# Optimization experiments

Hardware: AMD Instinct MI355X
Metric: run time of the kernel (lower is better)

The kernel has to match this reference:

```python
import jax, jax.numpy as jnp
import numpy as np

B_, L_, D_ = 4, 4096, 256
EXPAND = 2
DI_ = EXPAND * D_      # 512 inner channels
H_ = 8                 # heads
P_ = DI_ // H_         # 64 head dim
N_ = 16                # d_state
K_ = 3                 # depthwise conv kernel


def setup_inputs() -> dict:
    key = jax.random.key(0)
    ks = jax.random.split(key, 32)

    def n(i, shape, s=0.02):
        return jax.random.normal(ks[i], shape, jnp.float32) * s

    inp = {"inputs": jax.random.normal(ks[0], (B_, L_, D_), jnp.float32)}
    i = 1
    for pre in ("f_", "b_"):
        inp[pre + "in_proj_w"] = n(i, (2 * DI_, D_)); i += 1
        inp[pre + "in_proj_b"] = jnp.zeros((2 * DI_,), jnp.float32)
        inp[pre + "x_proj_w"] = n(i, (DI_ + 2 * H_ * N_, DI_)); i += 1
        inp[pre + "x_proj_b"] = jnp.zeros((DI_ + 2 * H_ * N_,), jnp.float32)
        inp[pre + "dt_bias"] = jnp.full((DI_,), -4.0, jnp.float32)  # softplus -> small dt
        inp[pre + "A_log"] = jnp.log(jnp.tile(jnp.arange(1, N_ + 1, dtype=jnp.float32), (DI_, 1)))
        inp[pre + "D_skip"] = jnp.ones((DI_,), jnp.float32)
        inp[pre + "out_proj_w"] = n(i, (D_, DI_)); i += 1
        inp[pre + "out_proj_b"] = jnp.zeros((D_,), jnp.float32)
    inp["norm_w"] = jnp.ones((D_,), jnp.float32)
    inp["norm_b"] = jnp.zeros((D_,), jnp.float32)
    inp["conv_w"] = n(20, (D_, 1, K_), 0.1)   # depthwise: (out_ch, in_ch/groups=1, k)
    inp["conv_b"] = jnp.zeros((D_,), jnp.float32)
    return inp


def _layernorm(x, w, b):
    m = x.mean(-1, keepdims=True)
    v = ((x - m) ** 2).mean(-1, keepdims=True)
    return (x - m) * jax.lax.rsqrt(v + 1e-5) * w + b


def _mh_ssm(x, in_w, in_b, xp_w, xp_b, dt_b, A_log, D_skip, out_w, out_b):
    # Multihead selective-scan SSM (Mamba-style). x: (B, L, D)
    Bsz, L, _ = x.shape
    xz = x @ in_w.T + in_b                      # (B, L, 2*DI)
    xi, z = jnp.split(xz, 2, axis=-1)
    xi = jax.nn.silu(xi)                        # (B, L, DI)
    proj = xi @ xp_w.T + xp_b                   # (B, L, DI + 2*H*N)
    dt = jax.nn.softplus(proj[..., :DI_] + dt_b)        # (B, L, DI)
    Bm = proj[..., DI_:DI_ + H_ * N_].reshape(Bsz, L, H_, N_)
    Cm = proj[..., DI_ + H_ * N_:].reshape(Bsz, L, H_, N_)
    A = -jnp.exp(A_log).reshape(H_, P_, N_)     # (H, P, N), negative
    x4 = xi.reshape(Bsz, L, H_, P_)
    dt4 = dt.reshape(Bsz, L, H_, P_)

    def step(h, t):
        xt, dtt, Bt, Ct = t                     # (B,H,P), (B,H,P), (B,H,N), (B,H,N)
        dA = jnp.exp(dtt[..., None] * A)        # (B,H,P,N)
        h = h * dA + dtt[..., None] * Bt[:, :, None, :] * xt[..., None]
        y = jnp.einsum('bhpn,bhn->bhp', h, Ct)
        return h, y

    xs = (x4.transpose(1, 0, 2, 3), dt4.transpose(1, 0, 2, 3),
          Bm.transpose(1, 0, 2, 3), Cm.transpose(1, 0, 2, 3))
    h0 = jnp.zeros((Bsz, H_, P_, N_), x.dtype)
    _, ys = jax.lax.scan(step, h0, xs)          # ys: (L,B,H,P)
    y = ys.transpose(1, 0, 2, 3).reshape(Bsz, L, DI_) + xi * D_skip
    y = y * jax.nn.silu(z)                      # gating
    return y @ out_w.T + out_b                  # (B, L, D)


def reference(inputs,
              f_in_proj_w, f_in_proj_b, f_x_proj_w, f_x_proj_b, f_dt_bias,
              f_A_log, f_D_skip, f_out_proj_w, f_out_proj_b,
              b_in_proj_w, b_in_proj_b, b_x_proj_w, b_x_proj_b, b_dt_bias,
              b_A_log, b_D_skip, b_out_proj_w, b_out_proj_b,
              norm_w, norm_b, conv_w, conv_b):
    # Cascaded bidirectional SSM: backward(flip(norm(forward(x)))) then flip back
    y1 = _mh_ssm(inputs, f_in_proj_w, f_in_proj_b, f_x_proj_w, f_x_proj_b,
                 f_dt_bias, f_A_log, f_D_skip, f_out_proj_w, f_out_proj_b)
    y1n = jnp.flip(_layernorm(y1, norm_w, norm_b), axis=1)
    y2 = _mh_ssm(y1n, b_in_proj_w, b_in_proj_b, b_x_proj_w, b_x_proj_b,
                 b_dt_bias, b_A_log, b_D_skip, b_out_proj_w, b_out_proj_b)
    out = jnp.flip(y2, axis=1)
    # locality branch: depthwise Conv1d (groups=C) + exact GELU
    xt = inputs.transpose(0, 2, 1)              # (B, C, L)
    c = jax.lax.conv_general_dilated(
        xt, conv_w, window_strides=(1,), padding=[(1, 1)],
        dimension_numbers=('NCH', 'OIH', 'NCH'), feature_group_count=D_)
    c = jax.nn.gelu(c + conv_b[None, :, None], approximate=False)
    return out + c.transpose(0, 2, 1)
```

## Files before the change

### kernel.cpp

```cpp
#include <hip/hip_runtime.h>
#include <hip/hip_bf16.h>
#include <cstdint>
#include <cstddef>

#define B_  4
#define L_  4096
#define D_  256
#define DI_ 512
#define H_  8
#define P_  64
#define N_  16
#define M_  (B_ * L_)
#define PROJ_ (DI_ + 2 * H_ * N_)

#define NC_ 128
#define CL_ (L_ / NC_)
#define NSEQ_ (B_ * H_ * P_ * N_)
#define LOG2E_ 1.4426950408889634f

typedef __bf16 bf16x8 __attribute__((ext_vector_type(8)));
typedef float f32x4 __attribute__((ext_vector_type(4)));

__device__ __forceinline__ void cp16_lds(const __hip_bfloat16* g, short* lds) {
    __builtin_amdgcn_global_load_lds(
        (const __attribute__((address_space(1))) void*)g,
        (__attribute__((address_space(3))) void*)lds, 16, 0, 0);
}

#define FS0 (M_ * D_)
#define FS1 (2 * DI_ * D_)
#define FS2 (PROJ_ * DI_)
#define FS3 (D_ * DI_)
#define FC1 (FS0 + FS1)
#define FC2 (FC1 + FS2)
#define FC3 (FC2 + FS3)
#define FC4 (FC3 + FS1)
#define FC5 (FC4 + FS2)
#define FC6 (FC5 + FS3)

__launch_bounds__(256)
__global__ void f2b_all(const float* __restrict__ i0, const float* __restrict__ i1,
                        const float* __restrict__ i2, const float* __restrict__ i3,
                        const float* __restrict__ i4, const float* __restrict__ i5,
                        const float* __restrict__ i6,
                        __hip_bfloat16* o0, __hip_bfloat16* o1, __hip_bfloat16* o2,
                        __hip_bfloat16* o3, __hip_bfloat16* o4, __hip_bfloat16* o5,
                        __hip_bfloat16* o6) {
    for (int idx = blockIdx.x * 256 + threadIdx.x; idx < FC6; idx += gridDim.x * 256) {
        const float* s; __hip_bfloat16* d; int off;
        if (idx < FS0)      { s = i0; d = o0; off = idx; }
        else if (idx < FC1) { s = i1; d = o1; off = idx - FS0; }
        else if (idx < FC2) { s = i2; d = o2; off = idx - FC1; }
        else if (idx < FC3) { s = i3; d = o3; off = idx - FC2; }
        else if (idx < FC4) { s = i4; d = o4; off = idx - FC3; }
        else if (idx < FC5) { s = i5; d = o5; off = idx - FC4; }
        else                { s = i6; d = o6; off = idx - FC5; }
        d[off] = __float2bfloat16(s[off]);
    }
}

template <int EPI>
__launch_bounds__(256)
__global__ void gemm_mfma(const __hip_bfloat16* __restrict__ A,
                          const __hip_bfloat16* __restrict__ W,
                          const float* __restrict__ bias, int Kv,
                          __hip_bfloat16* __restrict__ zb,
                          __hip_bfloat16* __restrict__ obf,
                          const float* __restrict__ aux) {
    __shared__ short As[128 * 64];
    __shared__ short Bs[128 * 64];
    const int tid = threadIdx.x;
    const int lane = tid & 63;
    const int wave = tid >> 6;
    const int bm = blockIdx.x * 128;
    const int bn = blockIdx.y * 128;
    const int wm = (wave >> 1) * 64;
    const int wn = (wave & 1) * 64;

    f32x4 acc[4][4];
#pragma unroll
    for (int i = 0; i < 4; ++i)
#pragma unroll
        for (int j = 0; j < 4; ++j) acc[i][j] = (f32x4)0.f;

    const int srow = lane >> 3;
    const int ssegx = ((lane & 7) ^ srow) * 8;
    const __hip_bfloat16* gA0 = A + (size_t)(bm + wave * 32 + srow) * Kv + ssegx;
    const __hip_bfloat16* gB0 = W + (size_t)(bn + wave * 32 + srow) * Kv + ssegx;
    short* lA0 = As + (wave * 32) * 64;
    short* lB0 = Bs + (wave * 32) * 64;

    const int fr = lane & 15;
    const int kq = lane >> 4;

    for (int k0 = 0; k0 < Kv; k0 += 64) {
#pragma unroll
        for (int rb = 0; rb < 4; ++rb) {
            cp16_lds(gA0 + (size_t)(rb * 8) * Kv + k0, lA0 + rb * 8 * 64);
            cp16_lds(gB0 + (size_t)(rb * 8) * Kv + k0, lB0 + rb * 8 * 64);
        }
        __syncthreads();
#pragma unroll
        for (int ks = 0; ks < 2; ++ks) {
            const int kgg = ks * 4 + kq;
            const int kslot = (kgg ^ (fr & 7)) * 8;
            bf16x8 af[4], bv[4];
#pragma unroll
            for (int i = 0; i < 4; ++i)
                af[i] = *reinterpret_cast<const bf16x8*>(
                    &As[(wm + i * 16 + fr) * 64 + kslot]);
#pragma unroll
            for (int j = 0; j < 4; ++j)
                bv[j] = *reinterpret_cast<const bf16x8*>(
                    &Bs[(wn + j * 16 + fr) * 64 + kslot]);
#pragma unroll
            for (int i = 0; i < 4; ++i)
#pragma unroll
                for (int j = 0; j < 4; ++j)
                    acc[i][j] = __builtin_amdgcn_mfma_f32_16x16x32_bf16(
                        af[i], bv[j], acc[i][j], 0, 0, 0);
        }
        __syncthreads();
    }

    const int n16 = lane & 15;
    const int r4 = (lane >> 4) * 4;
#pragma unroll
    for (int i = 0; i < 4; ++i) {
#pragma unroll
        for (int j = 0; j < 4; ++j) {
            const int cg = bn + wn + j * 16 + n16;
            const float bb = bias[cg];
#pragma unroll
            for (int v = 0; v < 4; ++v) {
                const int r = bm + wm + i * 16 + r4 + v;
                float val = acc[i][j][v] + bb;
                if (EPI == 1) {
                    if (cg < DI_) {
                        val = val / (1.f + __expf(-val));
                        obf[(size_t)r * DI_ + cg] = __float2bfloat16(val);
                    } else {
                        zb[(size_t)r * DI_ + cg - DI_] = __float2bfloat16(val);
                    }
                } else {
                    if (cg < DI_) {
                        const float x = val + aux[cg];
                        val = (x > 20.f) ? x : __logf(1.f + __expf(x));
                    }
                    obf[(size_t)r * PROJ_ + cg] = __float2bfloat16(val);
                }
            }
        }
    }
}

__launch_bounds__(256)
__global__ void gemm64_convout(const __hip_bfloat16* __restrict__ A,
                               const __hip_bfloat16* __restrict__ W,
                               const float* __restrict__ bias, int Kv,
                               float* __restrict__ out0,
                               const float* __restrict__ cw,
                               const float* __restrict__ cb,
                               const float* __restrict__ cinp) {
    __shared__ short As[64 * 64];
    __shared__ short Bs[64 * 64];
    const int tid = threadIdx.x;
    const int lane = tid & 63;
    const int wave = tid >> 6;
    const int bm = blockIdx.x * 64;
    const int bn = blockIdx.y * 64;
    const int wm = (wave >> 1) * 32;
    const int wn = (wave & 1) * 32;

    f32x4 acc[2][2];
#pragma unroll
    for (int i = 0; i < 2; ++i)
#pragma unroll
        for (int j = 0; j < 2; ++j) acc[i][j] = (f32x4)0.f;

    const int srow = lane >> 3;
    const int ssegx = ((lane & 7) ^ srow) * 8;
    const __hip_bfloat16* gA0 = A + (size_t)(bm + wave * 16 + srow) * Kv + ssegx;
    const __hip_bfloat16* gB0 = W + (size_t)(bn + wave * 16 + srow) * Kv + ssegx;
    short* lA0 = As + (wave * 16) * 64;
    short* lB0 = Bs + (wave * 16) * 64;

    const int fr = lane & 15;
    const int kq = lane >> 4;

    for (int k0 = 0; k0 < Kv; k0 += 64) {
#pragma unroll
        for (int rb = 0; rb < 2; ++rb) {
            cp16_lds(gA0 + (size_t)(rb * 8) * Kv + k0, lA0 + rb * 8 * 64);
            cp16_lds(gB0 + (size_t)(rb * 8) * Kv + k0, lB0 + rb * 8 * 64);
        }
        __syncthreads();
#pragma unroll
        for (int ks = 0; ks < 2; ++ks) {
            const int kgg = ks * 4 + kq;
            const int kslot = (kgg ^ (fr & 7)) * 8;
            bf16x8 af[2], bv[2];
#pragma unroll
            for (int i = 0; i < 2; ++i)
                af[i] = *reinterpret_cast<const bf16x8*>(
                    &As[(wm + i * 16 + fr) * 64 + kslot]);
#pragma unroll
            for (int j = 0; j < 2; ++j)
                bv[j] = *reinterpret_cast<const bf16x8*>(
                    &Bs[(wn + j * 16 + fr) * 64 + kslot]);
#pragma unroll
            for (int i = 0; i < 2; ++i)
#pragma unroll
                for (int j = 0; j < 2; ++j)
                    acc[i][j] = __builtin_amdgcn_mfma_f32_16x16x32_bf16(
                        af[i], bv[j], acc[i][j], 0, 0, 0);
        }
        __syncthreads();
    }

    const int n16 = lane & 15;
    const int r4 = (lane >> 4) * 4;
#pragma unroll
    for (int i = 0; i < 2; ++i) {
#pragma unroll
        for (int j = 0; j < 2; ++j) {
            const int cg = bn + wn + j * 16 + n16;
            const float bb = bias[cg];
#pragma unroll
            for (int v = 0; v < 4; ++v) {
                const int r = bm + wm + i * 16 + r4 + v;
                float val = acc[i][j][v] + bb;
                const int b = r >> 12;
                const int l = r & (L_ - 1);
                const int lo = L_ - 1 - l;
                const size_t base = ((size_t)(b << 12) + lo) * 256 + cg;
                float cv = fmaf(cinp[base], cw[cg * 3 + 1], cb[cg]);
                if (lo > 0) cv = fmaf(cinp[base - 256], cw[cg * 3 + 0], cv);
                if (lo + 1 < L_) cv = fmaf(cinp[base + 256], cw[cg * 3 + 2], cv);
                const float g = 0.5f * cv * (1.f + erff(cv * 0.70710678118654752f));
                out0[base] = val + g;
            }
        }
    }
}

__launch_bounds__(256)
__global__ void gemm_out_ln(const __hip_bfloat16* __restrict__ A,
                            const __hip_bfloat16* __restrict__ W,
                            const float* __restrict__ bias,
                            const float* __restrict__ lnw,
                            const float* __restrict__ lnb,
                            __hip_bfloat16* __restrict__ outb) {
    __shared__ short As[64 * 64];
    __shared__ short Ws[256 * 64];
    __shared__ float rs[2][4][64];
    const int tid = threadIdx.x;
    const int lane = tid & 63;
    const int wave = tid >> 6;
    const int bm = blockIdx.x * 64;
    const int Kv = DI_;

    f32x4 acc[4][4];
#pragma unroll
    for (int i = 0; i < 4; ++i)
#pragma unroll
        for (int j = 0; j < 4; ++j) acc[i][j] = (f32x4)0.f;

    const int srow = lane >> 3;
    const int ssegx = ((lane & 7) ^ srow) * 8;
    const __hip_bfloat16* gA0 = A + (size_t)(bm + wave * 16 + srow) * Kv + ssegx;
    const __hip_bfloat16* gW0 = W + (size_t)(wave * 64 + srow) * Kv + ssegx;
    short* lA0 = As + (wave * 16) * 64;
    short* lW0 = Ws + (wave * 64) * 64;

    const int fr = lane & 15;
    const int kq = lane >> 4;

    for (int k0 = 0; k0 < Kv; k0 += 64) {
#pragma unroll
        for (int rb = 0; rb < 2; ++rb)
            cp16_lds(gA0 + (size_t)(rb * 8) * Kv + k0, lA0 + rb * 8 * 64);
#pragma unroll
        for (int rb = 0; rb < 8; ++rb)
            cp16_lds(gW0 + (size_t)(rb * 8) * Kv + k0, lW0 + rb * 8 * 64);
        __syncthreads();
#pragma unroll
        for (int ks = 0; ks < 2; ++ks) {
            const int kgg = ks * 4 + kq;
            const int kslot = (kgg ^ (fr & 7)) * 8;
            bf16x8 af[4], bv[4];
#pragma unroll
            for (int i = 0; i < 4; ++i)
                af[i] = *reinterpret_cast<const bf16x8*>(
                    &As[(i * 16 + fr) * 64 + kslot]);
#pragma unroll
            for (int j = 0; j < 4; ++j)
                bv[j] = *reinterpret_cast<const bf16x8*>(
                    &Ws[(wave * 64 + j * 16 + fr) * 64 + kslot]);
#pragma unroll
            for (int i = 0; i < 4; ++i)
#pragma unroll
                for (int j = 0; j < 4; ++j)
                    acc[i][j] = __builtin_amdgcn_mfma_f32_16x16x32_bf16(
                        af[i], bv[j], acc[i][j], 0, 0, 0);
        }
        __syncthreads();
    }

    const int n16 = lane & 15;
    const int r4 = (lane >> 4) * 4;
#pragma unroll
    for (int j = 0; j < 4; ++j) {
        const float bb = bias[wave * 64 + j * 16 + n16];
#pragma unroll
        for (int i = 0; i < 4; ++i)
#pragma unroll
            for (int v = 0; v < 4; ++v) acc[i][j][v] += bb;
    }

#pragma unroll
    for (int i = 0; i < 4; ++i) {
#pragma unroll
        for (int v = 0; v < 4; ++v) {
            float s = 0.f, s2 = 0.f;
#pragma unroll
            for (int j = 0; j < 4; ++j) {
                const float t = acc[i][j][v];
                s += t; s2 = fmaf(t, t, s2);
            }
            s += __shfl_xor(s, 1); s2 += __shfl_xor(s2, 1);
            s += __shfl_xor(s, 2); s2 += __shfl_xor(s2, 2);
            s += __shfl_xor(s, 4); s2 += __shfl_xor(s2, 4);
            s += __shfl_xor(s, 8); s2 += __shfl_xor(s2, 8);
            if (n16 == 0) {
                rs[0][wave][i * 16 + r4 + v] = s;
                rs[1][wave][i * 16 + r4 + v] = s2;
            }
        }
    }
    __syncthreads();

#pragma unroll
    for (int i = 0; i < 4; ++i) {
#pragma unroll
        for (int v = 0; v < 4; ++v) {
            const int row = i * 16 + r4 + v;
            const float ts = rs[0][0][row] + rs[0][1][row] + rs[0][2][row] + rs[0][3][row];
            const float ts2 = rs[1][0][row] + rs[1][1][row] + rs[1][2][row] + rs[1][3][row];
            const float mean = ts * (1.f / 256.f);
            const float var = ts2 * (1.f / 256.f) - mean * mean;
            const float inv = rsqrtf(var + 1e-5f);
            const int rg = bm + row;
            const int b = rg >> 12;
            const int l = rg & (L_ - 1);
            const size_t drow = (size_t)((b << 12) + (L_ - 1 - l)) * 256;
#pragma unroll
            for (int j = 0; j < 4; ++j) {
                const int cg = wave * 64 + j * 16 + n16;
                const float o = (acc[i][j][v] - mean) * inv * lnw[cg] + lnb[cg];
                outb[drow + cg] = __float2bfloat16(o);
            }
        }
    }
}

__device__ __forceinline__ bool a_is_arith(const float* A2) {
    bool ok = true;
#pragma unroll
    for (int n = 1; n < N_; ++n)
        ok = ok && (fabsf(A2[n] - (float)(n + 1) * A2[0]) <= 1e-4f * fabsf(A2[n]));
    return ok;
}

__launch_bounds__(256)
__global__ void scan_chunk_state(const __hip_bfloat16* __restrict__ xi,
                                 const __hip_bfloat16* __restrict__ projb,
                                 const float* __restrict__ A_log,
                                 float* __restrict__ sS,
                                 float* __restrict__ st_hend) {
    __shared__ float bsh[4][CL_][16];
    const int bh = blockIdx.x;
    const int b = bh >> 3;
    const int h = bh & 7;
    const int lane = threadIdx.x & 63;
    const int wave = threadIdx.x >> 6;
    const int chunk = blockIdx.y * 4 + wave;
    const int t0 = chunk * CL_;
    const int c = h * P_ + lane;
    const int bOff = DI_ + h * N_;

    {
        const int stp = lane >> 1;
        const int half = (lane & 1) * 8;
        const __hip_bfloat16* src =
            projb + ((size_t)b * L_ + t0 + stp) * PROJ_ + bOff + half;
        const bf16x8 v = *reinterpret_cast<const bf16x8*>(src);
        float4* dst = reinterpret_cast<float4*>(&bsh[wave][stp][half]);
        dst[0] = make_float4((float)v[0], (float)v[1], (float)v[2], (float)v[3]);
        dst[1] = make_float4((float)v[4], (float)v[5], (float)v[6], (float)v[7]);
    }

    float A2[N_], hs[N_];
#pragma unroll
    for (int n = 0; n < N_; ++n) {
        A2[n] = -__expf(A_log[c * N_ + n]) * LOG2E_;
        hs[n] = 0.f;
    }
    const bool fast = a_is_arith(A2);

    const __hip_bfloat16* pDt = projb + ((size_t)b * L_ + t0) * PROJ_ + c;
    const __hip_bfloat16* px = xi + ((size_t)b * L_ + t0) * DI_ + c;
    float S = 0.f;

    if (fast) {
        float dtb[2][4], xb[2][4];
#pragma unroll
        for (int i = 0; i < 4; ++i) {
            dtb[0][i] = __bfloat162float(pDt[(size_t)i * PROJ_]);
            xb[0][i] = __bfloat162float(px[(size_t)i * DI_]);
        }
#pragma unroll
        for (int k = 0; k < CL_ / 4; ++k) {
            const int cur = k & 1, nxt = cur ^ 1;
            if (k + 1 < CL_ / 4) {
#pragma unroll
                for (int i = 0; i < 4; ++i) {
                    dtb[nxt][i] = __bfloat162float(pDt[(size_t)((k + 1) * 4 + i) * PROJ_]);
                    xb[nxt][i] = __bfloat162float(px[(size_t)((k + 1) * 4 + i) * DI_]);
                }
            }
#pragma unroll
            for (int i = 0; i < 4; ++i) {
                const int t = k * 4 + i;
                const float dt_v = dtb[cur][i];
                const float dtx = dt_v * xb[cur][i];
                const float e1 = exp2f(dt_v * A2[0]);
                S += dt_v;
                const f32x4* bp = reinterpret_cast<const f32x4*>(&bsh[wave][t][0]);
                float dA = e1;
#pragma unroll
                for (int q = 0; q < 4; ++q) {
                    const f32x4 Bq = bp[q];
#pragma unroll
                    for (int j = 0; j < 4; ++j) {
                        hs[q * 4 + j] = fmaf(hs[q * 4 + j], dA, dtx * Bq[j]);
                        dA *= e1;
                    }
                }
            }
        }
    } else {
#pragma unroll 4
        for (int t = 0; t < CL_; ++t) {
            const float dt_v = __bfloat162float(pDt[(size_t)t * PROJ_]);
            const float xv = __bfloat162float(px[(size_t)t * DI_]);
            const float dtx = dt_v * xv;
            S += dt_v;
#pragma unroll
            for (int n = 0; n < N_; ++n) {
                const float dA = exp2f(dt_v * A2[n]);
                hs[n] = fmaf(hs[n], dA, dtx * bsh[wave][t][n]);
            }
        }
    }

    sS[(size_t)chunk * (B_ * DI_) + (size_t)(bh * P_ + lane)] = S;
    const size_t s0 = (size_t)chunk * NSEQ_ + ((size_t)(bh * P_ + lane)) * N_;
#pragma unroll
    for (int n = 0; n < N_; n += 4) {
        *reinterpret_cast<float4*>(st_hend + s0 + n) =
            make_float4(hs[n], hs[n + 1], hs[n + 2], hs[n + 3]);
    }
}

__launch_bounds__(128)
__global__ void scan_combine(const float* __restrict__ sS,
                             const float* __restrict__ A_log,
                             float* __restrict__ st_prod,
                             const float* __restrict__ st_hend) {
    const int s = blockIdx.x * 128 + threadIdx.x;
    const int seqc = s >> 4;
    const int n = s & 15;
    const int cA = seqc & (DI_ - 1);
    const float A2n = -__expf(A_log[cA * N_ + n]) * LOG2E_;
    float H = 0.f;
#pragma unroll 8
    for (int k = 0; k < NC_; ++k) {
        const size_t o = (size_t)k * NSEQ_ + s;
        const float Pv = exp2f(A2n * sS[(size_t)k * (B_ * DI_) + seqc]);
        const float Ev = st_hend[o];
        st_prod[o] = H;
        H = fmaf(Pv, H, Ev);
    }
}

__launch_bounds__(256)
__global__ void scan_chunk_out(const __hip_bfloat16* __restrict__ xi,
                               const __hip_bfloat16* __restrict__ z,
                               const __hip_bfloat16* __restrict__ projb,
                               const float* __restrict__ A_log,
                               const float* __restrict__ D_skip,
                               const float* __restrict__ st_hin,
                               __hip_bfloat16* __restrict__ yg) {
    __shared__ float bc[4][CL_][32];
    const int bh = blockIdx.x;
    const int b = bh >> 3;
    const int h = bh & 7;
    const int lane = threadIdx.x & 63;
    const int wave = threadIdx.x >> 6;
    const int chunk = blockIdx.y * 4 + wave;
    const int t0 = chunk * CL_;
    const int c = h * P_ + lane;
    const int bOff = DI_ + h * N_;
    const int cOff = DI_ + H_ * N_ + h * N_;

    {
#pragma unroll
        for (int r = 0; r < 2; ++r) {
            const int g = r * 64 + lane;
            const int stp = g >> 2;
            const int q = g & 3;
            const int soff = (q < 2) ? (bOff + q * 8) : (cOff + (q - 2) * 8);
            const __hip_bfloat16* src =
                projb + ((size_t)b * L_ + t0 + stp) * PROJ_ + soff;
            const bf16x8 v = *reinterpret_cast<const bf16x8*>(src);
            float4* dst = reinterpret_cast<float4*>(&bc[wave][stp][q * 8]);
            dst[0] = make_float4((float)v[0], (float)v[1], (float)v[2], (float)v[3]);
            dst[1] = make_float4((float)v[4], (float)v[5], (float)v[6], (float)v[7]);
        }
    }

    float A2[N_], hs[N_];
    const size_t s0 = (size_t)chunk * NSEQ_ + ((size_t)(bh * P_ + lane)) * N_;
#pragma unroll
    for (int n = 0; n < N_; n += 4) {
        const float4 h4 = *reinterpret_cast<const float4*>(st_hin + s0 + n);
        hs[n] = h4.x; hs[n + 1] = h4.y; hs[n + 2] = h4.z; hs[n + 3] = h4.w;
    }
#pragma unroll
    for (int n = 0; n < N_; ++n)
        A2[n] = -__expf(A_log[c * N_ + n]) * LOG2E_;
    const bool fast = a_is_arith(A2);
    const float Dv = D_skip[c];

    const __hip_bfloat16* pDt = projb + ((size_t)b * L_ + t0) * PROJ_ + c;
    const __hip_bfloat16* px = xi + ((size_t)b * L_ + t0) * DI_ + c;
    const __hip_bfloat16* pz = z + ((size_t)b * L_ + t0) * DI_ + c;
    __hip_bfloat16* py = yg + ((size_t)b * L_ + t0) * DI_ + c;

    if (fast) {
        float dtb[2][4], xb[2][4], zb[2][4];
#pragma unroll
        for (int i = 0; i < 4; ++i) {
            dtb[0][i] = __bfloat162float(pDt[(size_t)i * PROJ_]);
            xb[0][i] = __bfloat162float(px[(size_t)i * DI_]);
            zb[0][i] = __bfloat162float(pz[(size_t)i * DI_]);
        }
#pragma unroll
        for (int k = 0; k < CL_ / 4; ++k) {
            const int cur = k & 1, nxt = cur ^ 1;
            if (k + 1 < CL_ / 4) {
#pragma unroll
                for (int i = 0; i < 4; ++i) {
                    const int t = (k + 1) * 4 + i;
                    dtb[nxt][i] = __bfloat162float(pDt[(size_t)t * PROJ_]);
                    xb[nxt][i] = __bfloat162float(px[(size_t)t * DI_]);
                    zb[nxt][i] = __bfloat162float(pz[(size_t)t * DI_]);
                }
            }
#pragma unroll
            for (int i = 0; i < 4; ++i) {
                const int t = k * 4 + i;
                const float dt_v = dtb[cur][i];
                const float xv = xb[cur][i];
                const float zv = zb[cur][i];
                const float dtx = dt_v * xv;
                const float e1 = exp2f(dt_v * A2[0]);
                const f32x4* bp = reinterpret_cast<const f32x4*>(&bc[wave][t][0]);
                float dA = e1;
                float y = 0.f;
#pragma unroll
                for (int q = 0; q < 4; ++q) {
                    const f32x4 Bq = bp[q];
                    const f32x4 Cq = bp[4 + q];
#pragma unroll
                    for (int j = 0; j < 4; ++j) {
                        hs[q * 4 + j] = fmaf(hs[q * 4 + j], dA, dtx * Bq[j]);
                        y = fmaf(hs[q * 4 + j], Cq[j], y);
                        dA *= e1;
                    }
                }
                const float g = zv / (1.f + __expf(-zv));
                py[(size_t)t * DI_] = __float2bfloat16((y + Dv * xv) * g);
            }
        }
    } else {
#pragma unroll 4
        for (int t = 0; t < CL_; ++t) {
            const float dt_v = __bfloat162float(pDt[(size_t)t * PROJ_]);
            const float xv = __bfloat162float(px[(size_t)t * DI_]);
            const float zv = __bfloat162float(pz[(size_t)t * DI_]);
            const float dtx = dt_v * xv;
            float y = 0.f;
#pragma unroll
            for (int n = 0; n < N_; ++n) {
                const float dA = exp2f(dt_v * A2[n]);
                hs[n] = fmaf(hs[n], dA, dtx * bc[wave][t][n]);
                y = fmaf(hs[n], bc[wave][t][16 + n], y);
            }
            const float g = zv / (1.f + __expf(-zv));
            py[(size_t)t * DI_] = __float2bfloat16((y + Dv * xv) * g);
        }
    }
}

extern "C" void kernel_launch(void* const* d_in, const int* in_sizes, int n_in,
                              void* d_out, int out_size, void* d_ws, size_t ws_size,
                              hipStream_t stream) {
    const float* inputs = (const float*)d_in[0];
    const float* f_in_w = (const float*)d_in[1];
    const float* f_in_b = (const float*)d_in[2];
    const float* f_xp_w = (const float*)d_in[3];
    const float* f_xp_b = (const float*)d_in[4];
    const float* f_dt_b = (const float*)d_in[5];
    const float* f_A = (const float*)d_in[6];
    const float* f_D = (const float*)d_in[7];
    const float* f_out_w = (const float*)d_in[8];
    const float* f_out_b = (const float*)d_in[9];
    const float* b_in_w = (const float*)d_in[10];
    const float* b_in_b = (const float*)d_in[11];
    const float* b_xp_w = (const float*)d_in[12];
    const float* b_xp_b = (const float*)d_in[13];
    const float* b_dt_b = (const float*)d_in[14];
    const float* b_A = (const float*)d_in[15];
    const float* b_D = (const float*)d_in[16];
    const float* b_out_w = (const float*)d_in[17];
    const float* b_out_b = (const float*)d_in[18];
    const float* norm_w = (const float*)d_in[19];
    const float* norm_b = (const float*)d_in[20];
    const float* conv_w = (const float*)d_in[21];
    const float* conv_b = (const float*)d_in[22];
    float* out = (float*)d_out;

    float* ws = (float*)d_ws;
    float* st_prod = ws;
    float* st_hend = st_prod + (size_t)NSEQ_ * NC_;
    float* zslot   = st_hend + (size_t)NSEQ_ * NC_;
    __hip_bfloat16* z_bf = (__hip_bfloat16*)zslot;
    float* pslot   = zslot + (size_t)M_ * DI_;
    __hip_bfloat16* proj_bf = (__hip_bfloat16*)pslot;
    float* y1      = pslot + (size_t)M_ * PROJ_;
    float* sS      = y1;
    __hip_bfloat16* xi_bf = (__hip_bfloat16*)(y1 + (size_t)M_ * D_);
    __hip_bfloat16* yg_bf = xi_bf + (size_t)M_ * DI_;
    __hip_bfloat16* a_bf  = yg_bf + (size_t)M_ * DI_;
    __hip_bfloat16* wpool = a_bf + (size_t)M_ * D_;
    __hip_bfloat16* f_in_wb  = wpool;
    __hip_bfloat16* f_xp_wb  = f_in_wb + 2 * DI_ * D_;
    __hip_bfloat16* f_out_wb = f_xp_wb + PROJ_ * DI_;
    __hip_bfloat16* b_in_wb  = f_out_wb + D_ * DI_;
    __hip_bfloat16* b_xp_wb  = b_in_wb + 2 * DI_ * D_;
    __hip_bfloat16* b_out_wb = b_xp_wb + PROJ_ * DI_;

    const dim3 blk(256);
    const dim3 g_in(M_ / 128, (2 * DI_) / 128);
    const dim3 g_xp(M_ / 128, PROJ_ / 128);
    const dim3 g_out64(M_ / 64, D_ / 64);
    const dim3 g_oln(M_ / 64);
    const dim3 g_chunk(B_ * H_, NC_ / 4);
    const dim3 g_comb(NSEQ_ / 128);
    const dim3 blk_comb(128);

    f2b_all<<<dim3(4096), blk, 0, stream>>>(inputs, f_in_w, f_xp_w, f_out_w,
                                            b_in_w, b_xp_w, b_out_w,
                                            a_bf, f_in_wb, f_xp_wb, f_out_wb,
                                            b_in_wb, b_xp_wb, b_out_wb);

    gemm_mfma<1><<<g_in, blk, 0, stream>>>(a_bf, f_in_wb, f_in_b, D_,
                                           z_bf, xi_bf, nullptr);
    gemm_mfma<2><<<g_xp, blk, 0, stream>>>(xi_bf, f_xp_wb, f_xp_b, DI_,
                                           nullptr, proj_bf, f_dt_b);
    scan_chunk_state<<<g_chunk, blk, 0, stream>>>(xi_bf, proj_bf, f_A,
                                                  sS, st_hend);
    scan_combine<<<g_comb, blk_comb, 0, stream>>>(sS, f_A, st_prod, st_hend);
    scan_chunk_out<<<g_chunk, blk, 0, stream>>>(xi_bf, z_bf, proj_bf, f_A, f_D,
                                                st_prod, yg_bf);
    gemm_out_ln<<<g_oln, blk, 0, stream>>>(yg_bf, f_out_wb, f_out_b,
                                           norm_w, norm_b, a_bf);

    gemm_mfma<1><<<g_in, blk, 0, stream>>>(a_bf, b_in_wb, b_in_b, D_,
                                           z_bf, xi_bf, nullptr);
    gemm_mfma<2><<<g_xp, blk, 0, stream>>>(xi_bf, b_xp_wb, b_xp_b, DI_,
                                           nullptr, proj_bf, b_dt_b);
    scan_chunk_state<<<g_chunk, blk, 0, stream>>>(xi_bf, proj_bf, b_A,
                                                  sS, st_hend);
    scan_combine<<<g_comb, blk_comb, 0, stream>>>(sS, b_A, st_prod, st_hend);
    scan_chunk_out<<<g_chunk, blk, 0, stream>>>(xi_bf, z_bf, proj_bf, b_A, b_D,
                                                st_prod, yg_bf);
    gemm64_convout<<<g_out64, blk, 0, stream>>>(yg_bf, b_out_wb, b_out_b, DI_,
                                                out, conv_w, conv_b, inputs);
}
```

Before: 384.3 us.

## Halve scan chunk count and store inter-chunk states in fp16

Reduces the number of scan chunks from 128 to 64, so each chunk is twice as long, and stores the per-chunk end states and combined prefix states as fp16 instead of fp32. The B/C staging loops are widened to fill the longer chunks. This cuts the state traffic between scan_chunk_state, scan_combine and scan_chunk_out by about four times and shortens the serial combine loop. In exchange each chunk's sequential loop runs longer with less parallelism, and fp16 state storage risks precision loss or overflow.

```diff
diff --git a/kernel.cpp b/kernel.cpp
--- a/kernel.cpp
+++ b/kernel.cpp
@@ -13,13 +13,14 @@
 #define M_  (B_ * L_)
 #define PROJ_ (DI_ + 2 * H_ * N_)
 
-#define NC_ 128
+#define NC_ 64
 #define CL_ (L_ / NC_)
 #define NSEQ_ (B_ * H_ * P_ * N_)
 #define LOG2E_ 1.4426950408889634f
 
 typedef __bf16 bf16x8 __attribute__((ext_vector_type(8)));
 typedef float f32x4 __attribute__((ext_vector_type(4)));
+typedef _Float16 f16x8 __attribute__((ext_vector_type(8)));
 
 __device__ __forceinline__ void cp16_lds(const __hip_bfloat16* g, short* lds) {
     __builtin_amdgcn_global_load_lds(
@@ -377,7 +378,7 @@
                                  const __hip_bfloat16* __restrict__ projb,
                                  const float* __restrict__ A_log,
                                  float* __restrict__ sS,
-                                 float* __restrict__ st_hend) {
+                                 _Float16* __restrict__ st_hend) {
     __shared__ float bsh[4][CL_][16];
     const int bh = blockIdx.x;
     const int b = bh >> 3;
@@ -390,14 +391,18 @@
     const int bOff = DI_ + h * N_;
 
     {
-        const int stp = lane >> 1;
-        const int half = (lane & 1) * 8;
-        const __hip_bfloat16* src =
-            projb + ((size_t)b * L_ + t0 + stp) * PROJ_ + bOff + half;
-        const bf16x8 v = *reinterpret_cast<const bf16x8*>(src);
-        float4* dst = reinterpret_cast<float4*>(&bsh[wave][stp][half]);
-        dst[0] = make_float4((float)v[0], (float)v[1], (float)v[2], (float)v[3]);
-        dst[1] = make_float4((float)v[4], (float)v[5], (float)v[6], (float)v[7]);
+#pragma unroll
+        for (int r = 0; r < 2; ++r) {
+            const int g = r * 64 + lane;
+            const int stp = g >> 1;
+            const int half = (g & 1) * 8;
+            const __hip_bfloat16* src =
+                projb + ((size_t)b * L_ + t0 + stp) * PROJ_ + bOff + half;
+            const bf16x8 v = *reinterpret_cast<const bf16x8*>(src);
+            float4* dst = reinterpret_cast<float4*>(&bsh[wave][stp][half]);
+            dst[0] = make_float4((float)v[0], (float)v[1], (float)v[2], (float)v[3]);
+            dst[1] = make_float4((float)v[4], (float)v[5], (float)v[6], (float)v[7]);
+        }
     }
 
     float A2[N_], hs[N_];
@@ -466,18 +471,18 @@
 
     sS[(size_t)chunk * (B_ * DI_) + (size_t)(bh * P_ + lane)] = S;
     const size_t s0 = (size_t)chunk * NSEQ_ + ((size_t)(bh * P_ + lane)) * N_;
-#pragma unroll
-    for (int n = 0; n < N_; n += 4) {
-        *reinterpret_cast<float4*>(st_hend + s0 + n) =
-            make_float4(hs[n], hs[n + 1], hs[n + 2], hs[n + 3]);
-    }
+    f16x8 h0, h1;
+#pragma unroll
+    for (int j = 0; j < 8; ++j) { h0[j] = (_Float16)hs[j]; h1[j] = (_Float16)hs[8 + j]; }
+    *reinterpret_cast<f16x8*>(st_hend + s0) = h0;
+    *reinterpret_cast<f16x8*>(st_hend + s0 + 8) = h1;
 }
 
 __launch_bounds__(128)
 __global__ void scan_combine(const float* __restrict__ sS,
                              const float* __restrict__ A_log,
-                             float* __restrict__ st_prod,
-                             const float* __restrict__ st_hend) {
+                             _Float16* __restrict__ st_prod,
+                             const _Float16* __restrict__ st_hend) {
     const int s = blockIdx.x * 128 + threadIdx.x;
     const int seqc = s >> 4;
     const int n = s & 15;
@@ -488,8 +493,8 @@
     for (int k = 0; k < NC_; ++k) {
         const size_t o = (size_t)k * NSEQ_ + s;
         const float Pv = exp2f(A2n * sS[(size_t)k * (B_ * DI_) + seqc]);
-        const float Ev = st_hend[o];
-        st_prod[o] = H;
+        const float Ev = (float)st_hend[o];
+        st_prod[o] = (_Float16)H;
         H = fmaf(Pv, H, Ev);
     }
 }
@@ -500,7 +505,7 @@
                                const __hip_bfloat16* __restrict__ projb,
                                const float* __restrict__ A_log,
                                const float* __restrict__ D_skip,
-                               const float* __restrict__ st_hin,
+                               const _Float16* __restrict__ st_hin,
                                __hip_bfloat16* __restrict__ yg) {
     __shared__ float bc[4][CL_][32];
     const int bh = blockIdx.x;
@@ -516,7 +521,7 @@
 
     {
 #pragma unroll
-        for (int r = 0; r < 2; ++r) {
+        for (int r = 0; r < 4; ++r) {
             const int g = r * 64 + lane;
             const int stp = g >> 2;
             const int q = g & 3;
@@ -532,10 +537,11 @@
 
     float A2[N_], hs[N_];
     const size_t s0 = (size_t)chunk * NSEQ_ + ((size_t)(bh * P_ + lane)) * N_;
-#pragma unroll
-    for (int n = 0; n < N_; n += 4) {
-        const float4 h4 = *reinterpret_cast<const float4*>(st_hin + s0 + n);
-        hs[n] = h4.x; hs[n + 1] = h4.y; hs[n + 2] = h4.z; hs[n + 3] = h4.w;
+    {
+        const f16x8 a0 = *reinterpret_cast<const f16x8*>(st_hin + s0);
+        const f16x8 a1 = *reinterpret_cast<const f16x8*>(st_hin + s0 + 8);
+#pragma unroll
+        for (int j = 0; j < 8; ++j) { hs[j] = (float)a0[j]; hs[8 + j] = (float)a1[j]; }
     }
 #pragma unroll
     for (int n = 0; n < N_; ++n)
@@ -643,9 +649,10 @@
     float* out = (float*)d_out;
 
     float* ws = (float*)d_ws;
-    float* st_prod = ws;
-    float* st_hend = st_prod + (size_t)NSEQ_ * NC_;
-    float* zslot   = st_hend + (size_t)NSEQ_ * NC_;
+    _Float16* st_prod = (_Float16*)ws;
+    float* slot1 = ws + (size_t)NSEQ_ * 128;
+    _Float16* st_hend = (_Float16*)slot1;
+    float* zslot   = slot1 + (size_t)NSEQ_ * 128;
     __hip_bfloat16* z_bf = (__hip_bfloat16*)zslot;
     float* pslot   = zslot + (size_t)M_ * DI_;
     __hip_bfloat16* proj_bf = (__hip_bfloat16*)pslot;
```

After: 364.7 us. -5.1%, faster.
